# Kernel optimization log

Hardware: AMD Instinct MI355X
Metric: run time of the kernel (lower is better)

The kernel has to match this reference:

```python
import jax, jax.numpy as jnp
import numpy as np

EPS_DIST = 1e-8   # matches 1.0/(dist + 1e-08) in the torch module
NEG_SLOPE = 0.2   # deep_gcns act_layer leakyrelu default
BN_EPS = 1e-5


def setup_inputs() -> dict:
    key = jax.random.key(0)
    ks = jax.random.split(key, 6)
    B, N, M = 8, 2048, 8192
    C, C_skip = 512, 256
    C_in = C + C_skip          # 768
    H1, H2 = 512, 256          # up_conv_nn = [768, 512, 256]
    pos = jax.random.normal(ks[0], (B, N, 3), dtype=jnp.float32)
    pos_skip = jax.random.normal(ks[1], (B, M, 3), dtype=jnp.float32)
    x = jax.random.normal(ks[2], (B, C, N), dtype=jnp.float32)
    x_skip = jax.random.normal(ks[3], (B, C_skip, M), dtype=jnp.float32)
    W1 = jax.random.normal(ks[4], (H1, C_in), dtype=jnp.float32) * (1.0 / np.sqrt(C_in))
    W2 = jax.random.normal(ks[5], (H2, H1), dtype=jnp.float32) * (1.0 / np.sqrt(H1))
    return {
        "pos": pos, "pos_skip": pos_skip, "x": x, "x_skip": x_skip,
        "W1": W1, "gamma1": jnp.ones((H1,), jnp.float32), "beta1": jnp.zeros((H1,), jnp.float32),
        "W2": W2, "gamma2": jnp.ones((H2,), jnp.float32), "beta2": jnp.zeros((H2,), jnp.float32),
    }


def _three_nn(query, ref):
    # query: [B, M, 3], ref: [B, N, 3] -> dist [B, M, 3], idx [B, M, 3]
    q2 = jnp.sum(query * query, axis=-1)                 # [B, M]
    r2 = jnp.sum(ref * ref, axis=-1)                     # [B, N]
    d2 = q2[:, :, None] + r2[:, None, :] - 2.0 * jnp.einsum('bmd,bnd->bmn', query, ref)
    neg_d2, idx = jax.lax.top_k(-d2, 3)                  # 3 smallest squared dists
    dist = jnp.sqrt(jnp.maximum(-neg_d2, 0.0))           # tp.three_nn returns L2 distance
    return dist, idx


def _three_interpolate(x, idx, weight):
    # x: [B, C, N], idx: [B, M, 3], weight: [B, M, 3] -> [B, C, M]
    xT = jnp.transpose(x, (0, 2, 1))                     # [B, N, C]
    gathered = jax.vmap(lambda f, i: f[i])(xT, idx)      # [B, M, 3, C]
    return jnp.einsum('bmkc,bmk->bcm', gathered, weight)


def _bn_act(h, gamma, beta):
    # training-mode BatchNorm1d over (batch, points) + LeakyReLU
    mean = jnp.mean(h, axis=(0, 2), keepdims=True)
    var = jnp.mean((h - mean) ** 2, axis=(0, 2), keepdims=True)
    h = (h - mean) * jax.lax.rsqrt(var + BN_EPS)
    h = h * gamma[None, :, None] + beta[None, :, None]
    return jnp.where(h >= 0, h, NEG_SLOPE * h)


def reference(pos, pos_skip, x, x_skip, W1, gamma1, beta1, W2, gamma2, beta2):
    # 3-NN of each fine point (pos_skip) among coarse points (pos)
    dist, idx = _three_nn(pos_skip, pos)
    dist_recip = 1.0 / (dist + EPS_DIST)
    norm = jnp.sum(dist_recip, axis=2, keepdims=True)
    weight = dist_recip / norm                           # [B, M, 3]
    interpolated = _three_interpolate(x, idx, weight)    # [B, C, M]
    feats = jnp.concatenate([interpolated, x_skip], axis=1)  # [B, C+C_skip, M]
    # MLP: Conv1d(k=1, bias=False) -> BN -> LeakyReLU, twice
    h = jnp.einsum('oi,bim->bom', W1, feats)
    h = _bn_act(h, gamma1, beta1)
    h = jnp.einsum('oi,bim->bom', W2, h)
    h = _bn_act(h, gamma2, beta2)
    return h  # [B, 256, M]
```

## Files before the change

### kernel.cpp

```cpp
#include <hip/hip_runtime.h>
#include <stdint.h>

#define B_    8
#define N_    2048
#define M_    8192
#define C_    512
#define CSK   256
#define CIN   768
#define H1C   512
#define H2C   256
#define NCOL  65536
typedef unsigned short u16;
typedef __attribute__((ext_vector_type(8))) short  s16x8;
typedef __attribute__((ext_vector_type(4))) float  f32x4;

__device__ inline u16 f2bf(float f) {
    unsigned u = __float_as_uint(f);
    unsigned r = (u + 0x7fffu + ((u >> 16) & 1u)) >> 16;
    return (u16)r;
}
__device__ inline float bflo(unsigned u) { return __uint_as_float(u << 16); }
__device__ inline float bfhi(unsigned u) { return __uint_as_float(u & 0xffff0000u); }

__global__ __launch_bounds__(256) void cvt_bf16_k(const float* __restrict__ in,
                                                  u16* __restrict__ out, int n4) {
    const int i = blockIdx.x * 256 + threadIdx.x;
    if (i >= n4) return;
    const float4 v = *(const float4*)(in + (size_t)i * 4);
    u16 o[4] = {f2bf(v.x), f2bf(v.y), f2bf(v.z), f2bf(v.w)};
    *(uint2*)(out + (size_t)i * 4) = *(uint2*)o;
}

__device__ inline void ins3(float d, int n,
                            float& d0, int& i0, float& d1, int& i1,
                            float& d2, int& i2) {
    const bool lt0 = d < d0, lt1 = d < d1, lt2 = d < d2;
    const float nd2 = lt1 ? d1 : (lt2 ? d : d2);
    const int   ni2 = lt1 ? i1 : (lt2 ? n : i2);
    const float nd1 = lt0 ? d0 : (lt1 ? d : d1);
    const int   ni1 = lt0 ? i0 : (lt1 ? n : i1);
    const float nd0 = lt0 ? d : d0;
    const int   ni0 = lt0 ? n : i0;
    d0 = nd0; d1 = nd1; d2 = nd2; i0 = ni0; i1 = ni1; i2 = ni2;
}

__global__ __launch_bounds__(256) void knn_kernel(const float* __restrict__ pos,
                                                  const float* __restrict__ pos_skip,
                                                  int* __restrict__ idx_out,
                                                  float* __restrict__ w_out) {
    __shared__ float rpx[N_], rpy[N_], rpz[N_];
    const int b = blockIdx.y;
    const int tid = threadIdx.x;
    for (int t = tid; t < N_ * 3; t += 256) {
        const float v = pos[(size_t)b * N_ * 3 + t];
        const int n = t / 3, k = t - n * 3;
        if (k == 0) rpx[n] = v; else if (k == 1) rpy[n] = v; else rpz[n] = v;
    }
    __syncthreads();

    const int q = tid >> 3;
    const int part = tid & 7;
    const int m = blockIdx.x * 32 + q;
    const size_t qoff = ((size_t)b * M_ + m) * 3;
    const float qx = pos_skip[qoff], qy = pos_skip[qoff + 1], qz = pos_skip[qoff + 2];

    float d0 = 1e30f, d1 = 1e30f, d2 = 1e30f;
    int i0 = 0, i1 = 0, i2 = 0;
#pragma unroll 4
    for (int i = 0; i < 64; ++i) {
        const int n = part * 4 + i * 32;
        const float4 xx = *(const float4*)&rpx[n];
        const float4 yy = *(const float4*)&rpy[n];
        const float4 zz = *(const float4*)&rpz[n];
        float dd[4];
        {
            const float dx = qx - xx.x, dy = qy - yy.x, dz = qz - zz.x;
            dd[0] = dx * dx + dy * dy + dz * dz;
        }
        {
            const float dx = qx - xx.y, dy = qy - yy.y, dz = qz - zz.y;
            dd[1] = dx * dx + dy * dy + dz * dz;
        }
        {
            const float dx = qx - xx.z, dy = qy - yy.z, dz = qz - zz.z;
            dd[2] = dx * dx + dy * dy + dz * dz;
        }
        {
            const float dx = qx - xx.w, dy = qy - yy.w, dz = qz - zz.w;
            dd[3] = dx * dx + dy * dy + dz * dz;
        }
        ins3(dd[0], n + 0, d0, i0, d1, i1, d2, i2);
        ins3(dd[1], n + 1, d0, i0, d1, i1, d2, i2);
        ins3(dd[2], n + 2, d0, i0, d1, i1, d2, i2);
        ins3(dd[3], n + 3, d0, i0, d1, i1, d2, i2);
    }

#pragma unroll
    for (int xm = 1; xm <= 4; xm <<= 1) {
        const float od0 = __shfl_xor(d0, xm), od1 = __shfl_xor(d1, xm), od2 = __shfl_xor(d2, xm);
        const int   oi0 = __shfl_xor(i0, xm), oi1 = __shfl_xor(i1, xm), oi2 = __shfl_xor(i2, xm);
        ins3(od0, oi0, d0, i0, d1, i1, d2, i2);
        ins3(od1, oi1, d0, i0, d1, i1, d2, i2);
        ins3(od2, oi2, d0, i0, d1, i1, d2, i2);
    }

    if (part == 0) {
        const float r0 = 1.0f / (sqrtf(d0) + 1e-8f);
        const float r1 = 1.0f / (sqrtf(d1) + 1e-8f);
        const float r2 = 1.0f / (sqrtf(d2) + 1e-8f);
        const float inv = 1.0f / (r0 + r1 + r2);
        const size_t o = ((size_t)b * M_ + m) * 3;
        idx_out[o] = i0; idx_out[o + 1] = i1; idx_out[o + 2] = i2;
        w_out[o] = r0 * inv; w_out[o + 1] = r1 * inv; w_out[o + 2] = r2 * inv;
    }
}

__global__ __launch_bounds__(256) void transpose_x(const float* __restrict__ x,
                                                   u16* __restrict__ xT) {
    __shared__ float t[32][33];
    const int tx = threadIdx.x & 31, ty = threadIdx.x >> 5;
    const int n0 = blockIdx.x * 32, c0 = blockIdx.y * 32, b = blockIdx.z;
#pragma unroll
    for (int r = 0; r < 4; ++r) {
        const int c = c0 + ty + r * 8;
        t[ty + r * 8][tx] = x[((size_t)b * C_ + c) * N_ + n0 + tx];
    }
    __syncthreads();
#pragma unroll
    for (int r = 0; r < 4; ++r) {
        const int n = n0 + ty + r * 8;
        xT[((size_t)b * N_ + n) * C_ + c0 + tx] = f2bf(t[tx][ty + r * 8]);
    }
}

__global__ __launch_bounds__(256) void feats_skip(const float* __restrict__ xs,
                                                  u16* __restrict__ Feats) {
    __shared__ float t[32][33];
    const int tx = threadIdx.x & 31, ty = threadIdx.x >> 5;
    const int m0 = blockIdx.x * 32, c0 = blockIdx.y * 32, b = blockIdx.z;
#pragma unroll
    for (int r = 0; r < 4; ++r) {
        const int c = c0 + ty + r * 8;
        t[ty + r * 8][tx] = xs[((size_t)b * CSK + c) * M_ + m0 + tx];
    }
    __syncthreads();
#pragma unroll
    for (int r = 0; r < 4; ++r) {
        const int m = m0 + ty + r * 8;
        Feats[((size_t)b * M_ + m) * CIN + C_ + c0 + tx] = f2bf(t[tx][ty + r * 8]);
    }
}

__device__ inline unsigned interp_pk(unsigned a, unsigned b, unsigned c,
                                     float w0, float w1, float w2) {
    const float lo = w0 * bflo(a) + w1 * bflo(b) + w2 * bflo(c);
    const float hi = w0 * bfhi(a) + w1 * bfhi(b) + w2 * bfhi(c);
    return (unsigned)f2bf(lo) | ((unsigned)f2bf(hi) << 16);
}
__global__ __launch_bounds__(256) void feats_interp(const u16* __restrict__ xT,
                                                    const int* __restrict__ idx,
                                                    const float* __restrict__ w,
                                                    u16* __restrict__ Feats) {
    const int b = blockIdx.y;
    const int lane = threadIdx.x & 63, wv = threadIdx.x >> 6;
    for (int t = 0; t < 16; ++t) {
        const int m = blockIdx.x * 64 + wv * 16 + t;
        const size_t col = (size_t)b * M_ + m;
        const int i0 = idx[col * 3], i1 = idx[col * 3 + 1], i2 = idx[col * 3 + 2];
        const float w0 = w[col * 3], w1 = w[col * 3 + 1], w2 = w[col * 3 + 2];
        const uint4 a = *(const uint4*)(xT + ((size_t)b * N_ + i0) * C_ + lane * 8);
        const uint4 c = *(const uint4*)(xT + ((size_t)b * N_ + i1) * C_ + lane * 8);
        const uint4 d = *(const uint4*)(xT + ((size_t)b * N_ + i2) * C_ + lane * 8);
        uint4 r;
        r.x = interp_pk(a.x, c.x, d.x, w0, w1, w2);
        r.y = interp_pk(a.y, c.y, d.y, w0, w1, w2);
        r.z = interp_pk(a.z, c.z, d.z, w0, w1, w2);
        r.w = interp_pk(a.w, c.w, d.w, w0, w1, w2);
        *(uint4*)(Feats + col * CIN + lane * 8) = r;
    }
}

__device__ inline void stage_tile(u16* lds, const u16* gbase, int ld,
                                  int lane, int wv) {
#pragma unroll
    for (int jj = 0; jj < 2; ++jj) {
        const int chunk = jj * 4 + wv;
        const int row = chunk * 16 + (lane >> 2);
        const int bir = (lane & 3) * 16;
        const char* g = (const char*)gbase + (size_t)row * (ld * 2) + bir;
        __builtin_amdgcn_global_load_lds(
            (const __attribute__((address_space(1))) void*)g,
            (__attribute__((address_space(3))) void*)((char*)lds + chunk * 1024),
            16, 0, 0);
    }
}

__global__ __launch_bounds__(256) void gemm1(const u16* __restrict__ A,
                                             const u16* __restrict__ Bm,
                                             u16* __restrict__ H1,
                                             float* __restrict__ ps1,
                                             float* __restrict__ pq1) {
    __shared__ __attribute__((aligned(16))) u16 As[128 * 32];
    __shared__ __attribute__((aligned(16))) u16 Bs[128 * 32];
    __shared__ float lsum[2][128], lsq[2][128];
    const int tid = threadIdx.x;
    const int lane = tid & 63, wv = tid >> 6;
    const int wr = wv >> 1, wc = wv & 1;
    const int l15 = lane & 15, l4 = lane >> 4;
    const int rowM0 = blockIdx.y * 128, colN0 = blockIdx.x * 128;
    f32x4 acc[4][4] = {};
    const u16* Ab = A  + (size_t)rowM0 * CIN;
    const u16* Bb = Bm + (size_t)colN0 * CIN;

    for (int k0 = 0; k0 < CIN; k0 += 32) {
        stage_tile(As, Ab + k0, CIN, lane, wv);
        stage_tile(Bs, Bb + k0, CIN, lane, wv);
        __syncthreads();
        s16x8 af[4], bfr[4];
#pragma unroll
        for (int i = 0; i < 4; ++i)
            af[i] = *(const s16x8*)&As[(wr * 64 + i * 16 + l15) * 32 + l4 * 8];
#pragma unroll
        for (int j = 0; j < 4; ++j)
            bfr[j] = *(const s16x8*)&Bs[(wc * 64 + j * 16 + l15) * 32 + l4 * 8];
#pragma unroll
        for (int i = 0; i < 4; ++i)
#pragma unroll
            for (int j = 0; j < 4; ++j)
                acc[i][j] = __builtin_amdgcn_mfma_f32_16x16x32_bf16(bfr[j], af[i], acc[i][j], 0, 0, 0);
        __syncthreads();
    }

#pragma unroll
    for (int i = 0; i < 4; ++i) {
        const int o = rowM0 + wr * 64 + i * 16 + l15;
#pragma unroll
        for (int j = 0; j < 4; ++j) {
            const int colb = colN0 + wc * 64 + j * 16 + l4 * 4;
#pragma unroll
            for (int r = 0; r < 4; ++r)
                H1[(size_t)(colb + r) * H1C + o] = f2bf(acc[i][j][r]);
        }
    }

#pragma unroll
    for (int i = 0; i < 4; ++i) {
        float s = 0.f, q = 0.f;
#pragma unroll
        for (int j = 0; j < 4; ++j)
#pragma unroll
            for (int r = 0; r < 4; ++r) {
                const float v = acc[i][j][r];
                s += v; q += v * v;
            }
        s += __shfl_xor(s, 16); q += __shfl_xor(q, 16);
        s += __shfl_xor(s, 32); q += __shfl_xor(q, 32);
        if ((lane & 48) == 0) {
            lsum[wc][wr * 64 + i * 16 + l15] = s;
            lsq [wc][wr * 64 + i * 16 + l15] = q;
        }
    }
    __syncthreads();
    if (tid < 128) {
        const float S = lsum[0][tid] + lsum[1][tid];
        const float Q = lsq[0][tid] + lsq[1][tid];
        ps1[(size_t)(rowM0 + tid) * 512 + blockIdx.x] = S;
        pq1[(size_t)(rowM0 + tid) * 512 + blockIdx.x] = Q;
    }
}

__global__ __launch_bounds__(256) void bn1_final(const float* __restrict__ ps,
                                                 const float* __restrict__ pq,
                                                 const float* __restrict__ gamma,
                                                 const float* __restrict__ beta,
                                                 float* __restrict__ sc,
                                                 float* __restrict__ sh) {
    const int o = blockIdx.x;
    const int t = threadIdx.x;
    float S = ps[(size_t)o * 512 + t] + ps[(size_t)o * 512 + 256 + t];
    float Q = pq[(size_t)o * 512 + t] + pq[(size_t)o * 512 + 256 + t];
    __shared__ float rs[256], rq[256];
    rs[t] = S; rq[t] = Q;
    __syncthreads();
    for (int st = 128; st > 0; st >>= 1) {
        if (t < st) { rs[t] += rs[t + st]; rq[t] += rq[t + st]; }
        __syncthreads();
    }
    if (t == 0) {
        const float mean = rs[0] * (1.0f / NCOL);
        const float var  = fmaxf(rq[0] * (1.0f / NCOL) - mean * mean, 0.f);
        const float is   = rsqrtf(var + 1e-5f);
        const float s    = gamma[o] * is;
        sc[o] = s;
        sh[o] = beta[o] - mean * s;
    }
}

__global__ __launch_bounds__(256) void bn1_apply(u16* __restrict__ H1,
                                                 const float* __restrict__ sc,
                                                 const float* __restrict__ sh) {
    const size_t g = (size_t)blockIdx.x * 256 + threadIdx.x;
    const int og = (int)(g & 63) * 8;
    const size_t col = g >> 6;
    u16* p = H1 + col * H1C + og;
    uint4 v = *(const uint4*)p;
    unsigned u[4] = {v.x, v.y, v.z, v.w};
    const float4 s0 = *(const float4*)(sc + og), s1 = *(const float4*)(sc + og + 4);
    const float4 h0 = *(const float4*)(sh + og), h1 = *(const float4*)(sh + og + 4);
    const float scv[8] = {s0.x, s0.y, s0.z, s0.w, s1.x, s1.y, s1.z, s1.w};
    const float shv[8] = {h0.x, h0.y, h0.z, h0.w, h1.x, h1.y, h1.z, h1.w};
    unsigned r[4];
#pragma unroll
    for (int e = 0; e < 4; ++e) {
        float f0 = fmaf(bflo(u[e]), scv[e * 2], shv[e * 2]);
        float f1 = fmaf(bfhi(u[e]), scv[e * 2 + 1], shv[e * 2 + 1]);
        f0 = f0 >= 0.f ? f0 : 0.2f * f0;
        f1 = f1 >= 0.f ? f1 : 0.2f * f1;
        r[e] = (unsigned)f2bf(f0) | ((unsigned)f2bf(f1) << 16);
    }
    *(uint4*)p = make_uint4(r[0], r[1], r[2], r[3]);
}

__device__ inline void stage2(char* ldsbase, const u16* gsrc, int k0,
                              int lane, int wv) {
#pragma unroll
    for (int h = 0; h < 2; ++h) {
        const int p_loc = h * 128 + wv * 16 + (lane >> 2);
        const u16* g = gsrc + (size_t)p_loc * H1C + k0 + (lane & 3) * 8;
        __builtin_amdgcn_global_load_lds(
            (const __attribute__((address_space(1))) void*)g,
            (__attribute__((address_space(3))) void*)(ldsbase + (h * 512 + wv * 64) * 16),
            16, 0, 0);
    }
}

__global__ __launch_bounds__(512, 2) void gemm2(const u16* __restrict__ W2b,
                                                const u16* __restrict__ H1,
                                                float* __restrict__ out,
                                                float* __restrict__ ps2,
                                                float* __restrict__ pq2) {
    __shared__ __attribute__((aligned(16))) u16 As[2][256 * 32];
    __shared__ __attribute__((aligned(16))) u16 Bs[2][256 * 32];
    __shared__ float lsum[4][256], lsq[4][256];
    const int tid = threadIdx.x;
    const int lane = tid & 63, wv = tid >> 6;
    const int pgrp = wv & 1, cgrp = wv >> 1;
    const int l15 = lane & 15, l4 = lane >> 4;
    const int col0 = blockIdx.x * 256;
    const u16* Hb = H1 + (size_t)col0 * H1C;
    f32x4 acc[4][8] = {};

    stage2((char*)As[0], W2b, 0, lane, wv);
    stage2((char*)Bs[0], Hb, 0, lane, wv);
    __syncthreads();

    int cur = 0;
    for (int step = 0; step < 16; ++step) {
        if (step < 15) {
            stage2((char*)As[cur ^ 1], W2b, (step + 1) * 32, lane, wv);
            stage2((char*)Bs[cur ^ 1], Hb, (step + 1) * 32, lane, wv);
        }
        const u16* Ac = As[cur];
        const u16* Bc = Bs[cur];
        s16x8 af[8], bfr[4];
#pragma unroll
        for (int pf = 0; pf < 8; ++pf)
            af[pf] = *(const s16x8*)&Ac[(pgrp * 128 + pf * 16 + l15) * 32 + l4 * 8];
#pragma unroll
        for (int cf = 0; cf < 4; ++cf)
            bfr[cf] = *(const s16x8*)&Bc[(cgrp * 64 + cf * 16 + l15) * 32 + l4 * 8];
#pragma unroll
        for (int cf = 0; cf < 4; ++cf)
#pragma unroll
            for (int pf = 0; pf < 8; ++pf)
                acc[cf][pf] = __builtin_amdgcn_mfma_f32_16x16x32_bf16(bfr[cf], af[pf], acc[cf][pf], 0, 0, 0);
        __syncthreads();
        cur ^= 1;
    }

    const int bidx = col0 >> 13;
    const int mb   = col0 & (M_ - 1);
#pragma unroll
    for (int cf = 0; cf < 4; ++cf) {
#pragma unroll
        for (int pf = 0; pf < 8; ++pf) {
            const int p  = pgrp * 128 + pf * 16 + l15;
            const int mm = mb + cgrp * 64 + cf * 16 + l4 * 4;
            *(f32x4*)(out + (size_t)bidx * (H2C * M_) + (size_t)p * M_ + mm) = acc[cf][pf];
        }
    }

#pragma unroll
    for (int pf = 0; pf < 8; ++pf) {
        float s = 0.f, q = 0.f;
#pragma unroll
        for (int cf = 0; cf < 4; ++cf)
#pragma unroll
            for (int r = 0; r < 4; ++r) {
                const float v = acc[cf][pf][r];
                s += v; q += v * v;
            }
        s += __shfl_xor(s, 16); q += __shfl_xor(q, 16);
        s += __shfl_xor(s, 32); q += __shfl_xor(q, 32);
        if ((lane & 48) == 0) {
            lsum[cgrp][pgrp * 128 + pf * 16 + l15] = s;
            lsq [cgrp][pgrp * 128 + pf * 16 + l15] = q;
        }
    }
    __syncthreads();
    if (tid < 256) {
        const float S = lsum[0][tid] + lsum[1][tid] + lsum[2][tid] + lsum[3][tid];
        const float Q = lsq[0][tid] + lsq[1][tid] + lsq[2][tid] + lsq[3][tid];
        ps2[(size_t)tid * 256 + blockIdx.x] = S;
        pq2[(size_t)tid * 256 + blockIdx.x] = Q;
    }
}

__global__ __launch_bounds__(256) void bn2_final(const float* __restrict__ ps,
                                                 const float* __restrict__ pq,
                                                 const float* __restrict__ gamma,
                                                 const float* __restrict__ beta,
                                                 float* __restrict__ sc,
                                                 float* __restrict__ sh) {
    const int p = blockIdx.x;
    const int t = threadIdx.x;
    float S = ps[(size_t)p * 256 + t];
    float Q = pq[(size_t)p * 256 + t];
    __shared__ float rs[256], rq[256];
    rs[t] = S; rq[t] = Q;
    __syncthreads();
    for (int st = 128; st > 0; st >>= 1) {
        if (t < st) { rs[t] += rs[t + st]; rq[t] += rq[t + st]; }
        __syncthreads();
    }
    if (t == 0) {
        const float mean = rs[0] * (1.0f / NCOL);
        const float var  = fmaxf(rq[0] * (1.0f / NCOL) - mean * mean, 0.f);
        const float is   = rsqrtf(var + 1e-5f);
        const float s    = gamma[p] * is;
        sc[p] = s;
        sh[p] = beta[p] - mean * s;
    }
}

__global__ __launch_bounds__(256) void bn_apply2(float* __restrict__ out,
                                                 const float* __restrict__ sc,
                                                 const float* __restrict__ sh) {
    const size_t i = (size_t)blockIdx.x * 256 + threadIdx.x;
    const int p = (int)((i >> 13) & (H2C - 1));
    float v = out[i];
    v = fmaf(v, sc[p], sh[p]);
    out[i] = v >= 0.f ? v : 0.2f * v;
}

extern "C" void kernel_launch(void* const* d_in, const int* in_sizes, int n_in,
                              void* d_out, int out_size, void* d_ws, size_t ws_size,
                              hipStream_t stream) {
    const float* pos      = (const float*)d_in[0];
    const float* pos_skip = (const float*)d_in[1];
    const float* x        = (const float*)d_in[2];
    const float* x_skip   = (const float*)d_in[3];
    const float* W1       = (const float*)d_in[4];
    const float* gamma1   = (const float*)d_in[5];
    const float* beta1    = (const float*)d_in[6];
    const float* W2       = (const float*)d_in[7];
    const float* gamma2   = (const float*)d_in[8];
    const float* beta2    = (const float*)d_in[9];
    float* out = (float*)d_out;

    char* ws = (char*)d_ws;
    size_t off = 0;
    auto alloc = [&](size_t bytes) {
        void* p = ws + off;
        off = (off + bytes + 255) & ~(size_t)255;
        return p;
    };
    int*   idx   = (int*)  alloc((size_t)NCOL * 3 * sizeof(int));
    float* w     = (float*)alloc((size_t)NCOL * 3 * sizeof(float));
    u16*   xT    = (u16*)  alloc((size_t)B_ * N_ * C_ * sizeof(u16));
    u16*   W1b   = (u16*)  alloc((size_t)H1C * CIN * sizeof(u16));
    u16*   W2b   = (u16*)  alloc((size_t)H2C * H1C * sizeof(u16));
    u16*   Feats = (u16*)  alloc((size_t)NCOL * CIN * sizeof(u16));
    u16*   H1    = (u16*)  alloc((size_t)NCOL * H1C * sizeof(u16));
    float* ps1   = (float*)alloc((size_t)H1C * 512 * sizeof(float));
    float* pq1   = (float*)alloc((size_t)H1C * 512 * sizeof(float));
    float* ps2   = (float*)alloc((size_t)H2C * 256 * sizeof(float));
    float* pq2   = (float*)alloc((size_t)H2C * 256 * sizeof(float));
    float* sc1   = (float*)alloc(H1C * sizeof(float));
    float* sh1   = (float*)alloc(H1C * sizeof(float));
    float* sc2   = (float*)alloc(H2C * sizeof(float));
    float* sh2   = (float*)alloc(H2C * sizeof(float));

    cvt_bf16_k<<<(H1C * CIN / 4 + 255) / 256, 256, 0, stream>>>(W1, W1b, H1C * CIN / 4);
    cvt_bf16_k<<<(H2C * H1C / 4 + 255) / 256, 256, 0, stream>>>(W2, W2b, H2C * H1C / 4);
    knn_kernel<<<dim3(M_ / 32, B_), 256, 0, stream>>>(pos, pos_skip, idx, w);
    transpose_x<<<dim3(N_ / 32, C_ / 32, B_), 256, 0, stream>>>(x, xT);
    feats_interp<<<dim3(M_ / 64, B_), 256, 0, stream>>>(xT, idx, w, Feats);
    feats_skip<<<dim3(M_ / 32, CSK / 32, B_), 256, 0, stream>>>(x_skip, Feats);
    gemm1<<<dim3(NCOL / 128, H1C / 128), 256, 0, stream>>>(W1b, Feats, H1, ps1, pq1);
    bn1_final<<<H1C, 256, 0, stream>>>(ps1, pq1, gamma1, beta1, sc1, sh1);
    bn1_apply<<<(int)(((size_t)NCOL * H1C / 8) / 256), 256, 0, stream>>>(H1, sc1, sh1);
    gemm2<<<NCOL / 256, 512, 0, stream>>>(W2b, H1, out, ps2, pq2);
    bn2_final<<<H2C, 256, 0, stream>>>(ps2, pq2, gamma2, beta2, sc2, sh2);
    bn_apply2<<<(int)(((size_t)NCOL * H2C) / 256), 256, 0, stream>>>(out, sc2, sh2);
}
```

Before: 331.2 us.

## Fuse BN1 apply into GEMM2 B-load and widen GEMM1 K-tile with swizzled LDS

Removes the standalone bn1_apply pass by loading H1 tiles into registers in gemm2, applying the BN scale/shift and LeakyReLU, then writing the result to LDS. This avoids an extra read and write of the full 64 MB H1 buffer. gemm1 now stages 64-wide K tiles with an XOR-swizzled LDS layout to cut bank conflicts and halve the number of barriers. It also remaps the block index so that the 4 row blocks sharing a column tile are grouped, for better L2 reuse. The trade-off is that gemm2's B operand is now staged through registers instead of direct global-to-LDS loads, which adds VALU work and register pressure inside the main loop.

```diff
diff --git a/kernel.cpp b/kernel.cpp
--- a/kernel.cpp
+++ b/kernel.cpp
@@ -180,14 +180,14 @@
     }
 }
 
-__device__ inline void stage_tile(u16* lds, const u16* gbase, int ld,
-                                  int lane, int wv) {
-#pragma unroll
-    for (int jj = 0; jj < 2; ++jj) {
+__device__ inline void stage64(u16* lds, const char* gbase, int ld2,
+                               int lane, int wv) {
+    const int slot = (lane & 7) ^ (lane >> 3);
+#pragma unroll
+    for (int jj = 0; jj < 4; ++jj) {
         const int chunk = jj * 4 + wv;
-        const int row = chunk * 16 + (lane >> 2);
-        const int bir = (lane & 3) * 16;
-        const char* g = (const char*)gbase + (size_t)row * (ld * 2) + bir;
+        const int row = chunk * 8 + (lane >> 3);
+        const char* g = gbase + (size_t)row * ld2 + slot * 16;
         __builtin_amdgcn_global_load_lds(
             (const __attribute__((address_space(1))) void*)g,
             (__attribute__((address_space(3))) void*)((char*)lds + chunk * 1024),
@@ -200,34 +200,45 @@
                                              u16* __restrict__ H1,
                                              float* __restrict__ ps1,
                                              float* __restrict__ pq1) {
-    __shared__ __attribute__((aligned(16))) u16 As[128 * 32];
-    __shared__ __attribute__((aligned(16))) u16 Bs[128 * 32];
+    __shared__ __attribute__((aligned(16))) u16 As[128 * 64];
+    __shared__ __attribute__((aligned(16))) u16 Bs[128 * 64];
     __shared__ float lsum[2][128], lsq[2][128];
     const int tid = threadIdx.x;
     const int lane = tid & 63, wv = tid >> 6;
     const int wr = wv >> 1, wc = wv & 1;
     const int l15 = lane & 15, l4 = lane >> 4;
-    const int rowM0 = blockIdx.y * 128, colN0 = blockIdx.x * 128;
+    const int v = (blockIdx.x & 7) * 256 + (blockIdx.x >> 3);
+    const int rowblk = v & 3, colblk = v >> 2;
+    const int rowM0 = rowblk * 128, colN0 = colblk * 128;
     f32x4 acc[4][4] = {};
-    const u16* Ab = A  + (size_t)rowM0 * CIN;
-    const u16* Bb = Bm + (size_t)colN0 * CIN;
-
-    for (int k0 = 0; k0 < CIN; k0 += 32) {
-        stage_tile(As, Ab + k0, CIN, lane, wv);
-        stage_tile(Bs, Bb + k0, CIN, lane, wv);
+    const char* Ab = (const char*)(A  + (size_t)rowM0 * CIN);
+    const char* Bb = (const char*)(Bm + (size_t)colN0 * CIN);
+
+    for (int kt = 0; kt < CIN / 64; ++kt) {
+        stage64(As, Ab + kt * 128, CIN * 2, lane, wv);
+        stage64(Bs, Bb + kt * 128, CIN * 2, lane, wv);
         __syncthreads();
-        s16x8 af[4], bfr[4];
-#pragma unroll
-        for (int i = 0; i < 4; ++i)
-            af[i] = *(const s16x8*)&As[(wr * 64 + i * 16 + l15) * 32 + l4 * 8];
-#pragma unroll
-        for (int j = 0; j < 4; ++j)
-            bfr[j] = *(const s16x8*)&Bs[(wc * 64 + j * 16 + l15) * 32 + l4 * 8];
-#pragma unroll
-        for (int i = 0; i < 4; ++i)
-#pragma unroll
-            for (int j = 0; j < 4; ++j)
-                acc[i][j] = __builtin_amdgcn_mfma_f32_16x16x32_bf16(bfr[j], af[i], acc[i][j], 0, 0, 0);
+#pragma unroll
+        for (int ks = 0; ks < 2; ++ks) {
+            s16x8 af[4], bfr[4];
+#pragma unroll
+            for (int i = 0; i < 4; ++i) {
+                const int R = wr * 64 + i * 16 + l15;
+                const int s = ((ks << 2) | l4) ^ (R & 7);
+                af[i] = *(const s16x8*)((const char*)As + R * 128 + s * 16);
+            }
+#pragma unroll
+            for (int j = 0; j < 4; ++j) {
+                const int R = wc * 64 + j * 16 + l15;
+                const int s = ((ks << 2) | l4) ^ (R & 7);
+                bfr[j] = *(const s16x8*)((const char*)Bs + R * 128 + s * 16);
+            }
+#pragma unroll
+            for (int i = 0; i < 4; ++i)
+#pragma unroll
+                for (int j = 0; j < 4; ++j)
+                    acc[i][j] = __builtin_amdgcn_mfma_f32_16x16x32_bf16(bfr[j], af[i], acc[i][j], 0, 0, 0);
+        }
         __syncthreads();
     }
 
@@ -250,8 +261,8 @@
         for (int j = 0; j < 4; ++j)
 #pragma unroll
             for (int r = 0; r < 4; ++r) {
-                const float v = acc[i][j][r];
-                s += v; q += v * v;
+                const float vv = acc[i][j][r];
+                s += vv; q += vv * vv;
             }
         s += __shfl_xor(s, 16); q += __shfl_xor(q, 16);
         s += __shfl_xor(s, 32); q += __shfl_xor(q, 32);
@@ -264,8 +275,8 @@
     if (tid < 128) {
         const float S = lsum[0][tid] + lsum[1][tid];
         const float Q = lsq[0][tid] + lsq[1][tid];
-        ps1[(size_t)(rowM0 + tid) * 512 + blockIdx.x] = S;
-        pq1[(size_t)(rowM0 + tid) * 512 + blockIdx.x] = Q;
+        ps1[(size_t)(rowM0 + tid) * 512 + colblk] = S;
+        pq1[(size_t)(rowM0 + tid) * 512 + colblk] = Q;
     }
 }
 
@@ -296,69 +307,82 @@
     }
 }
 
-__global__ __launch_bounds__(256) void bn1_apply(u16* __restrict__ H1,
-                                                 const float* __restrict__ sc,
-                                                 const float* __restrict__ sh) {
-    const size_t g = (size_t)blockIdx.x * 256 + threadIdx.x;
-    const int og = (int)(g & 63) * 8;
-    const size_t col = g >> 6;
-    u16* p = H1 + col * H1C + og;
-    uint4 v = *(const uint4*)p;
-    unsigned u[4] = {v.x, v.y, v.z, v.w};
-    const float4 s0 = *(const float4*)(sc + og), s1 = *(const float4*)(sc + og + 4);
-    const float4 h0 = *(const float4*)(sh + og), h1 = *(const float4*)(sh + og + 4);
-    const float scv[8] = {s0.x, s0.y, s0.z, s0.w, s1.x, s1.y, s1.z, s1.w};
-    const float shv[8] = {h0.x, h0.y, h0.z, h0.w, h1.x, h1.y, h1.z, h1.w};
-    unsigned r[4];
-#pragma unroll
-    for (int e = 0; e < 4; ++e) {
-        float f0 = fmaf(bflo(u[e]), scv[e * 2], shv[e * 2]);
-        float f1 = fmaf(bfhi(u[e]), scv[e * 2 + 1], shv[e * 2 + 1]);
-        f0 = f0 >= 0.f ? f0 : 0.2f * f0;
-        f1 = f1 >= 0.f ? f1 : 0.2f * f1;
-        r[e] = (unsigned)f2bf(f0) | ((unsigned)f2bf(f1) << 16);
-    }
-    *(uint4*)p = make_uint4(r[0], r[1], r[2], r[3]);
-}
-
-__device__ inline void stage2(char* ldsbase, const u16* gsrc, int k0,
-                              int lane, int wv) {
+__device__ inline void stage2A(u16* dst, const u16* W2b, int k0,
+                               int lane, int wv) {
 #pragma unroll
     for (int h = 0; h < 2; ++h) {
         const int p_loc = h * 128 + wv * 16 + (lane >> 2);
-        const u16* g = gsrc + (size_t)p_loc * H1C + k0 + (lane & 3) * 8;
+        const u16* g = W2b + (size_t)p_loc * H1C + k0 + (lane & 3) * 8;
         __builtin_amdgcn_global_load_lds(
             (const __attribute__((address_space(1))) void*)g,
-            (__attribute__((address_space(3))) void*)(ldsbase + (h * 512 + wv * 64) * 16),
+            (__attribute__((address_space(3))) void*)((char*)dst + (h * 512 + wv * 64) * 16),
             16, 0, 0);
     }
 }
 
 __global__ __launch_bounds__(512, 2) void gemm2(const u16* __restrict__ W2b,
                                                 const u16* __restrict__ H1,
+                                                const float* __restrict__ sc1,
+                                                const float* __restrict__ sh1,
                                                 float* __restrict__ out,
                                                 float* __restrict__ ps2,
                                                 float* __restrict__ pq2) {
     __shared__ __attribute__((aligned(16))) u16 As[2][256 * 32];
     __shared__ __attribute__((aligned(16))) u16 Bs[2][256 * 32];
     __shared__ float lsum[4][256], lsq[4][256];
+    __shared__ float scs[512], shs[512];
     const int tid = threadIdx.x;
     const int lane = tid & 63, wv = tid >> 6;
     const int pgrp = wv & 1, cgrp = wv >> 1;
     const int l15 = lane & 15, l4 = lane >> 4;
     const int col0 = blockIdx.x * 256;
     const u16* Hb = H1 + (size_t)col0 * H1C;
+    const int kb = (lane & 3) * 8;
+    const int prow0 = wv * 16 + (lane >> 2);
     f32x4 acc[4][8] = {};
 
-    stage2((char*)As[0], W2b, 0, lane, wv);
-    stage2((char*)Bs[0], Hb, 0, lane, wv);
+    scs[tid] = sc1[tid];
+    shs[tid] = sh1[tid];
+
+    stage2A(As[0], W2b, 0, lane, wv);
+    uint4 nb0 = *(const uint4*)(Hb + (size_t)prow0 * H1C + kb);
+    uint4 nb1 = *(const uint4*)(Hb + (size_t)(prow0 + 128) * H1C + kb);
+    __syncthreads();
+
+    auto xformB = [&](int buf, uint4 b0, uint4 b1, int k0) {
+        const f32x4 s0v = *(const f32x4*)&scs[k0 + kb];
+        const f32x4 s1v = *(const f32x4*)&scs[k0 + kb + 4];
+        const f32x4 h0v = *(const f32x4*)&shs[k0 + kb];
+        const f32x4 h1v = *(const f32x4*)&shs[k0 + kb + 4];
+        const float sv[8] = {s0v[0], s0v[1], s0v[2], s0v[3], s1v[0], s1v[1], s1v[2], s1v[3]};
+        const float hv[8] = {h0v[0], h0v[1], h0v[2], h0v[3], h1v[0], h1v[1], h1v[2], h1v[3]};
+        uint4 bw[2] = {b0, b1};
+#pragma unroll
+        for (int h = 0; h < 2; ++h) {
+            unsigned uu[4] = {bw[h].x, bw[h].y, bw[h].z, bw[h].w};
+            unsigned rr[4];
+#pragma unroll
+            for (int e = 0; e < 4; ++e) {
+                float f0 = fmaf(bflo(uu[e]), sv[e * 2], hv[e * 2]);
+                float f1 = fmaf(bfhi(uu[e]), sv[e * 2 + 1], hv[e * 2 + 1]);
+                f0 = f0 >= 0.f ? f0 : 0.2f * f0;
+                f1 = f1 >= 0.f ? f1 : 0.2f * f1;
+                rr[e] = (unsigned)f2bf(f0) | ((unsigned)f2bf(f1) << 16);
+            }
+            *(uint4*)&Bs[buf][(size_t)(h * 512 + wv * 64 + lane) * 8] = make_uint4(rr[0], rr[1], rr[2], rr[3]);
+        }
+    };
+
+    xformB(0, nb0, nb1, 0);
     __syncthreads();
 
     int cur = 0;
     for (int step = 0; step < 16; ++step) {
         if (step < 15) {
-            stage2((char*)As[cur ^ 1], W2b, (step + 1) * 32, lane, wv);
-            stage2((char*)Bs[cur ^ 1], Hb, (step + 1) * 32, lane, wv);
+            const int k0 = (step + 1) * 32;
+            stage2A(As[cur ^ 1], W2b, k0, lane, wv);
+            nb0 = *(const uint4*)(Hb + (size_t)prow0 * H1C + k0 + kb);
+            nb1 = *(const uint4*)(Hb + (size_t)(prow0 + 128) * H1C + k0 + kb);
         }
         const u16* Ac = As[cur];
         const u16* Bc = Bs[cur];
@@ -374,6 +398,9 @@
 #pragma unroll
             for (int pf = 0; pf < 8; ++pf)
                 acc[cf][pf] = __builtin_amdgcn_mfma_f32_16x16x32_bf16(bfr[cf], af[pf], acc[cf][pf], 0, 0, 0);
+        if (step < 15) {
+            xformB(cur ^ 1, nb0, nb1, (step + 1) * 32);
+        }
         __syncthreads();
         cur ^= 1;
     }
@@ -397,8 +424,8 @@
         for (int cf = 0; cf < 4; ++cf)
 #pragma unroll
             for (int r = 0; r < 4; ++r) {
-                const float v = acc[cf][pf][r];
-                s += v; q += v * v;
+                const float vv = acc[cf][pf][r];
+                s += vv; q += vv * vv;
             }
         s += __shfl_xor(s, 16); q += __shfl_xor(q, 16);
         s += __shfl_xor(s, 32); q += __shfl_xor(q, 32);
@@ -497,10 +524,9 @@
     transpose_x<<<dim3(N_ / 32, C_ / 32, B_), 256, 0, stream>>>(x, xT);
     feats_interp<<<dim3(M_ / 64, B_), 256, 0, stream>>>(xT, idx, w, Feats);
     feats_skip<<<dim3(M_ / 32, CSK / 32, B_), 256, 0, stream>>>(x_skip, Feats);
-    gemm1<<<dim3(NCOL / 128, H1C / 128), 256, 0, stream>>>(W1b, Feats, H1, ps1, pq1);
+    gemm1<<<2048, 256, 0, stream>>>(W1b, Feats, H1, ps1, pq1);
     bn1_final<<<H1C, 256, 0, stream>>>(ps1, pq1, gamma1, beta1, sc1, sh1);
-    bn1_apply<<<(int)(((size_t)NCOL * H1C / 8) / 256), 256, 0, stream>>>(H1, sc1, sh1);
-    gemm2<<<NCOL / 256, 512, 0, stream>>>(W2b, H1, out, ps2, pq2);
+    gemm2<<<NCOL / 256, 512, 0, stream>>>(W2b, H1, sc1, sh1, out, ps2, pq2);
     bn2_final<<<H2C, 256, 0, stream>>>(ps2, pq2, gamma2, beta2, sc2, sh2);
     bn_apply2<<<(int)(((size_t)NCOL * H2C) / 256), 256, 0, stream>>>(out, sc2, sh2);
 }
```

After: 302.3 us. 8.7% less time.
